# Performance work log

Measured on AMD Instinct MI355X. Metric: run time of the kernel, lower is better.

## Reference

```python
import jax, jax.numpy as jnp
import numpy as np

EPS = 1e-5

def _layernorm(x, gamma, beta, axes):
    mean = jnp.mean(x, axis=axes, keepdims=True)
    var = jnp.var(x, axis=axes, keepdims=True)
    return (x - mean) * jax.lax.rsqrt(var + EPS) * gamma + beta

def setup_inputs() -> dict:
    key = jax.random.key(0)
    ks = jax.random.split(key, 14)
    B, N1, N2, D1, D2 = 128, 32, 32, 23, 13
    E, H, F = 72, 256, 128
    N = N1 + N2
    s = 0.05
    return {
        "x_a": jax.random.normal(ks[0], (B, N1, D1), jnp.float32),
        "x_b": jax.random.normal(ks[1], (B, N2, D2), jnp.float32),
        "W_a": jax.random.normal(ks[2], (D1, E), jnp.float32) * s,
        "b_a": jnp.zeros((E,), jnp.float32),
        "W_b": jax.random.normal(ks[3], (D2, E), jnp.float32) * s,
        "b_b": jnp.zeros((E,), jnp.float32),
        "ln0_g": jnp.ones((N, E), jnp.float32),
        "ln0_b": jnp.zeros((N, E), jnp.float32),
        "W_g": jax.random.normal(ks[4], (2 * E, H), jnp.float32) * s,
        "b_g": jnp.zeros((H,), jnp.float32),
        "lng_g": jnp.ones((H,), jnp.float32),
        "lng_b": jnp.zeros((H,), jnp.float32),
        "W_f": jax.random.normal(ks[5], (H, F), jnp.float32) * s,
        "b_f": jnp.zeros((F,), jnp.float32),
    }

def reference(x_a, x_b, W_a, b_a, W_b, b_b, ln0_g, ln0_b,
              W_g, b_g, lng_g, lng_b, W_f, b_f):
    # SplitEmbedding: per-group linear embed, concat along entity dim
    a = jnp.concatenate([x_a @ W_a + b_a, x_b @ W_b + b_b], axis=-2)  # [B, N, E]
    # LayerNorm over last two dims (num_entities, embed_dim) jointly
    a = _layernorm(a, ln0_g, ln0_b, axes=(-2, -1))
    B, N, E = a.shape
    # ij(): aij[b, i, j] = concat(a[b, i], a[b, j])  -> [B, N, N, 2E]
    ai = jnp.broadcast_to(a[:, :, None, :], (B, N, N, E))
    aj = jnp.broadcast_to(a[:, None, :, :], (B, N, N, E))
    aij = jnp.concatenate([ai, aj], axis=-1)
    # g: Linear(2E, H) + ELU, then LayerNorm(H)
    g = jax.nn.elu(aij @ W_g + b_g)  # [B, N, N, H]
    g = _layernorm(g, lng_g, lng_b, axes=(-1,))
    # sum over both pairwise dims
    s = jnp.sum(g, axis=(-3, -2))  # [B, H]
    # f: Linear(H, F) + ELU
    return jax.nn.elu(s @ W_f + b_f)  # [B, F]
```

## Files before the change

### kernel.cpp

```cpp
#include <hip/hip_runtime.h>
#include <hip/hip_bf16.h>

#define EPS 1e-5f
#define LOG2E 1.44269504088896f
#define LN2   0.69314718055995f

typedef float v2f __attribute__((ext_vector_type(2)));

#define OFF_ABAR 0
#define OFF_U    589824
#define OFF_V    2686976
#define OFF_PART 4784128

__device__ __forceinline__ float elu(float z) {
    return z > 0.f ? z : __expf(z) - 1.f;
}

__global__ __launch_bounds__(256) void k_embed_ln0(
    const float* __restrict__ xa, const float* __restrict__ xb,
    const float* __restrict__ Wa, const float* __restrict__ ba,
    const float* __restrict__ Wb, const float* __restrict__ bb,
    const float* __restrict__ g0, const float* __restrict__ b0,
    float* __restrict__ abar) {
    int b = blockIdx.x;
    int tid = threadIdx.x;
    __shared__ float S[3888];
    float* s_xa = S;
    float* s_xb = S + 736;
    float* s_Wa = S + 1152;
    float* s_Wb = S + 2808;
    float* s_ba = S + 3744;
    float* s_bb = S + 3816;
    for (int k = tid; k < 736;  k += 256) s_xa[k] = xa[b * 736 + k];
    for (int k = tid; k < 416;  k += 256) s_xb[k] = xb[b * 416 + k];
    for (int k = tid; k < 1656; k += 256) s_Wa[k] = Wa[k];
    for (int k = tid; k < 936;  k += 256) s_Wb[k] = Wb[k];
    if (tid < 72) { s_ba[tid] = ba[tid]; s_bb[tid] = bb[tid]; }
    __syncthreads();

    float vals[18];
    float s1 = 0.f, s2 = 0.f;
    #pragma unroll
    for (int m = 0; m < 18; ++m) {
        int k = tid + 256 * m;
        int e = k % 72;
        int n = k / 72;
        float acc;
        if (n < 32) {
            acc = s_ba[e];
            const float* x = s_xa + n * 23;
            #pragma unroll
            for (int d = 0; d < 23; ++d) acc = fmaf(x[d], s_Wa[d * 72 + e], acc);
        } else {
            acc = s_bb[e];
            const float* x = s_xb + (n - 32) * 13;
            #pragma unroll
            for (int d = 0; d < 13; ++d) acc = fmaf(x[d], s_Wb[d * 72 + e], acc);
        }
        vals[m] = acc;
        s1 += acc;
        s2 = fmaf(acc, acc, s2);
    }
    #pragma unroll
    for (int off = 32; off >= 1; off >>= 1) {
        s1 += __shfl_xor(s1, off, 64);
        s2 += __shfl_xor(s2, off, 64);
    }
    __shared__ float r1[4], r2[4];
    int w = tid >> 6;
    if ((tid & 63) == 0) { r1[w] = s1; r2[w] = s2; }
    __syncthreads();
    float t1 = r1[0] + r1[1] + r1[2] + r1[3];
    float t2 = r2[0] + r2[1] + r2[2] + r2[3];
    float mean = t1 * (1.f / 4608.f);
    float var  = fmaf(-mean, mean, t2 * (1.f / 4608.f));
    float rsq  = rsqrtf(var + EPS);
    float* ab = abar + b * 4608;
    #pragma unroll
    for (int m = 0; m < 18; ++m) {
        int k = tid + 256 * m;
        ab[k] = fmaf((vals[m] - mean) * rsq, g0[k], b0[k]);
    }
}

__global__ __launch_bounds__(256) void k_uv(
    const float* __restrict__ abar, const float* __restrict__ Wg,
    const float* __restrict__ bg,
    float* __restrict__ U, float* __restrict__ V) {
    int blk = blockIdx.x;
    int b = blk >> 3;
    int q = blk & 7;
    int h = threadIdx.x;
    __shared__ float sa[72 * 8];
    const float* src = abar + (b * 64 + q * 8) * 72;
    for (int k = threadIdx.x; k < 72 * 8; k += 256) {
        int e = k >> 3, n = k & 7;
        sa[k] = src[n * 72 + e];
    }
    __syncthreads();
    float u[8], v[8];
    #pragma unroll
    for (int n = 0; n < 8; ++n) { u[n] = 0.f; v[n] = 0.f; }
    #pragma unroll 6
    for (int e = 0; e < 72; ++e) {
        float wu = Wg[e * 256 + h];
        float wv = Wg[(72 + e) * 256 + h];
        const float4* sp = (const float4*)&sa[e * 8];
        #pragma unroll
        for (int n4 = 0; n4 < 2; ++n4) {
            float4 s4 = sp[n4];
            u[n4*4+0] = fmaf(s4.x, wu, u[n4*4+0]); v[n4*4+0] = fmaf(s4.x, wv, v[n4*4+0]);
            u[n4*4+1] = fmaf(s4.y, wu, u[n4*4+1]); v[n4*4+1] = fmaf(s4.y, wv, v[n4*4+1]);
            u[n4*4+2] = fmaf(s4.z, wu, u[n4*4+2]); v[n4*4+2] = fmaf(s4.z, wv, v[n4*4+2]);
            u[n4*4+3] = fmaf(s4.w, wu, u[n4*4+3]); v[n4*4+3] = fmaf(s4.w, wv, v[n4*4+3]);
        }
    }
    float bgh = bg[h];
    int base = (b * 64 + q * 8) * 256 + h;
    #pragma unroll
    for (int n = 0; n < 8; ++n) {
        U[base + n * 256] = u[n] + bgh;
        V[base + n * 256] = v[n];
    }
}

__global__ __launch_bounds__(256) void k_pair(
    const float* __restrict__ U, const float* __restrict__ V,
    float* __restrict__ part) {
    int blk = blockIdx.x;
    int b  = blk >> 5;
    int iq = (blk >> 2) & 7;
    int jq = blk & 3;
    int t  = threadIdx.x;
    int j16 = t >> 4;
    int hc  = t & 15;

    __shared__ float Us[16 * 256];

    const float* Ug = U + (size_t)(b * 64 + iq * 8) * 256;
    #pragma unroll
    for (int r = 0; r < 2; ++r) {
        int k = t * 4 + r * 1024;
        *(float4*)&Us[k] = *(const float4*)&Ug[k];
    }

    const float* Vrow = V + (size_t)(b * 64 + jq * 16 + j16) * 256;
    v2f v[8];
    #pragma unroll
    for (int c = 0; c < 4; ++c) {
        float4 v4 = *(const float4*)&Vrow[hc * 4 + 64 * c];
        v[2*c]   = (v2f){v4.x, v4.y};
        v[2*c+1] = (v2f){v4.z, v4.w};
    }

    __syncthreads();

    v2f acc[8];
    #pragma unroll
    for (int k = 0; k < 8; ++k) acc[k] = (v2f){0.f, 0.f};
    float macc = 0.f;

    #pragma unroll 2
    for (int i = 0; i < 8; ++i) {
        const float* ur = &Us[i * 256];
        v2f e[8];
        v2f s1v = (v2f){0.f, 0.f};
        v2f s2v = (v2f){0.f, 0.f};
        #pragma unroll
        for (int c = 0; c < 8; ++c) {
            float2 u2 = *(const float2*)&ur[hc * 4 + 32 * c + (c & 1) * 0];
            (void)u2;
        }
        #pragma unroll
        for (int c = 0; c < 4; ++c) {
            float4 u4 = *(const float4*)&ur[hc * 4 + 64 * c];
            v2f z0 = (v2f){u4.x, u4.y} + v[2*c];
            v2f z1 = (v2f){u4.z, u4.w} + v[2*c+1];
            v2f zl0 = z0 * (v2f){LOG2E, LOG2E};
            v2f zl1 = z1 * (v2f){LOG2E, LOG2E};
            v2f e0, e1;
            e0.x = zl0.x > 0.f ? z0.x : __builtin_amdgcn_exp2f(zl0.x) - 1.f;
            e0.y = zl0.y > 0.f ? z0.y : __builtin_amdgcn_exp2f(zl0.y) - 1.f;
            e1.x = zl1.x > 0.f ? z1.x : __builtin_amdgcn_exp2f(zl1.x) - 1.f;
            e1.y = zl1.y > 0.f ? z1.y : __builtin_amdgcn_exp2f(zl1.y) - 1.f;
            e[2*c] = e0; e[2*c+1] = e1;
            s1v += e0 + e1;
            s2v = e0 * e0 + s2v;
            s2v = e1 * e1 + s2v;
        }
        float s1 = s1v.x + s1v.y;
        float s2 = s2v.x + s2v.y;
        #pragma unroll
        for (int d = 1; d <= 8; d <<= 1) {
            s1 += __shfl_xor(s1, d, 64);
            s2 += __shfl_xor(s2, d, 64);
        }
        float mu  = s1 * (1.f / 256.f);
        float var = fmaf(-mu, mu, s2 * (1.f / 256.f));
        float rsq = rsqrtf(var + EPS);
        macc += mu * rsq;
        v2f r2 = (v2f){rsq, rsq};
        #pragma unroll
        for (int k = 0; k < 8; ++k) acc[k] = e[k] * r2 + acc[k];
    }
    v2f m2 = (v2f){macc, macc};
    #pragma unroll
    for (int k = 0; k < 8; ++k) acc[k] -= m2;

    __syncthreads();
    #pragma unroll
    for (int c = 0; c < 4; ++c)
        *(float4*)&Us[j16 * 256 + hc * 4 + 64 * c] =
            make_float4(acc[2*c].x, acc[2*c].y, acc[2*c+1].x, acc[2*c+1].y);
    __syncthreads();
    float r = 0.f;
    #pragma unroll
    for (int q = 0; q < 16; ++q) r += Us[q * 256 + t];
    part[(size_t)blk * 256 + t] = r;
}

__global__ __launch_bounds__(512) void k_out(
    const float* __restrict__ part,
    const float* __restrict__ lgg, const float* __restrict__ lgb,
    const float* __restrict__ Wf,  const float* __restrict__ bfb,
    float* __restrict__ out) {
    int b = blockIdx.x;
    int t = threadIdx.x;
    __shared__ float sh[256];
    __shared__ float ps[512];
    {
        int h = t & 255, pg = t >> 8;
        float s = 0.f;
        #pragma unroll
        for (int p = 0; p < 16; ++p)
            s += part[(size_t)(b * 32 + pg * 16 + p) * 256 + h];
        ps[t] = s;
    }
    __syncthreads();
    if (t < 256) sh[t] = fmaf(lgg[t], ps[t] + ps[t + 256], 4096.f * lgb[t]);
    __syncthreads();
    {
        int f = t & 127, hq = t >> 7;
        float acc = 0.f;
        #pragma unroll 8
        for (int h = hq * 64; h < hq * 64 + 64; ++h)
            acc = fmaf(sh[h], Wf[h * 128 + f], acc);
        ps[t] = acc;
    }
    __syncthreads();
    if (t < 128) {
        float r = ps[t] + ps[t + 128] + ps[t + 256] + ps[t + 384] + bfb[t];
        out[b * 128 + t] = r > 0.f ? r : __expf(r) - 1.f;
    }
}

extern "C" void kernel_launch(void* const* d_in, const int* in_sizes, int n_in,
                              void* d_out, int out_size, void* d_ws, size_t ws_size,
                              hipStream_t stream) {
    const float* xa  = (const float*)d_in[0];
    const float* xb  = (const float*)d_in[1];
    const float* Wa  = (const float*)d_in[2];
    const float* ba  = (const float*)d_in[3];
    const float* Wb  = (const float*)d_in[4];
    const float* bb  = (const float*)d_in[5];
    const float* g0  = (const float*)d_in[6];
    const float* b0  = (const float*)d_in[7];
    const float* Wg  = (const float*)d_in[8];
    const float* bg  = (const float*)d_in[9];
    const float* lgg = (const float*)d_in[10];
    const float* lgb = (const float*)d_in[11];
    const float* Wf  = (const float*)d_in[12];
    const float* bfb = (const float*)d_in[13];
    float* out = (float*)d_out;

    float* ws   = (float*)d_ws;
    float* abar = ws + OFF_ABAR;
    float* U    = ws + OFF_U;
    float* V    = ws + OFF_V;
    float* part = ws + OFF_PART;

    k_embed_ln0<<<128, 256, 0, stream>>>(xa, xb, Wa, ba, Wb, bb, g0, b0, abar);
    k_uv<<<1024, 256, 0, stream>>>(abar, Wg, bg, U, V);
    k_pair<<<4096, 256, 0, stream>>>(U, V, part);
    k_out<<<128, 512, 0, stream>>>(part, lgg, lgb, Wf, bfb, out);
}
```

Before: 145.0 us.

## Fuse embedding+LayerNorm into U/V projection kernel, recomputing per block

Merges the embedding/LN0 kernel into the U/V projection kernel. Each of the 1024 blocks recomputes the full per-batch embedding and LayerNorm statistics, then keeps only its 8 entities in shared memory. This removes one kernel launch and the global round trip of the normalized activations. In exchange the embedding work is done 8 times redundantly. It also deletes a dead load loop in the pair kernel.

```diff
diff --git a/kernel.cpp b/kernel.cpp
--- a/kernel.cpp
+++ b/kernel.cpp
@@ -16,15 +16,21 @@
     return z > 0.f ? z : __expf(z) - 1.f;
 }
 
-__global__ __launch_bounds__(256) void k_embed_ln0(
+__global__ __launch_bounds__(256) void k_embed_uv(
     const float* __restrict__ xa, const float* __restrict__ xb,
     const float* __restrict__ Wa, const float* __restrict__ ba,
     const float* __restrict__ Wb, const float* __restrict__ bb,
     const float* __restrict__ g0, const float* __restrict__ b0,
-    float* __restrict__ abar) {
-    int b = blockIdx.x;
+    const float* __restrict__ Wg, const float* __restrict__ bg,
+    float* __restrict__ U, float* __restrict__ V) {
+    int blk = blockIdx.x;
+    int b = blk >> 3;
+    int q = blk & 7;
     int tid = threadIdx.x;
+
     __shared__ float S[3888];
+    __shared__ float sa[72 * 8];
+    __shared__ float r1[4], r2[4];
     float* s_xa = S;
     float* s_xb = S + 736;
     float* s_Wa = S + 1152;
@@ -66,7 +72,6 @@
         s1 += __shfl_xor(s1, off, 64);
         s2 += __shfl_xor(s2, off, 64);
     }
-    __shared__ float r1[4], r2[4];
     int w = tid >> 6;
     if ((tid & 63) == 0) { r1[w] = s1; r2[w] = s2; }
     __syncthreads();
@@ -75,29 +80,20 @@
     float mean = t1 * (1.f / 4608.f);
     float var  = fmaf(-mean, mean, t2 * (1.f / 4608.f));
     float rsq  = rsqrtf(var + EPS);
-    float* ab = abar + b * 4608;
+
+    int n0 = q * 8;
     #pragma unroll
     for (int m = 0; m < 18; ++m) {
         int k = tid + 256 * m;
-        ab[k] = fmaf((vals[m] - mean) * rsq, g0[k], b0[k]);
-    }
-}
-
-__global__ __launch_bounds__(256) void k_uv(
-    const float* __restrict__ abar, const float* __restrict__ Wg,
-    const float* __restrict__ bg,
-    float* __restrict__ U, float* __restrict__ V) {
-    int blk = blockIdx.x;
-    int b = blk >> 3;
-    int q = blk & 7;
-    int h = threadIdx.x;
-    __shared__ float sa[72 * 8];
-    const float* src = abar + (b * 64 + q * 8) * 72;
-    for (int k = threadIdx.x; k < 72 * 8; k += 256) {
-        int e = k >> 3, n = k & 7;
-        sa[k] = src[n * 72 + e];
-    }
-    __syncthreads();
+        int dn = k / 72 - n0;
+        if ((unsigned)dn < 8u) {
+            int e = k % 72;
+            sa[e * 8 + dn] = fmaf((vals[m] - mean) * rsq, g0[k], b0[k]);
+        }
+    }
+    __syncthreads();
+
+    int h = tid;
     float u[8], v[8];
     #pragma unroll
     for (int n = 0; n < 8; ++n) { u[n] = 0.f; v[n] = 0.f; }
@@ -116,7 +112,7 @@
         }
     }
     float bgh = bg[h];
-    int base = (b * 64 + q * 8) * 256 + h;
+    int base = (b * 64 + n0) * 256 + h;
     #pragma unroll
     for (int n = 0; n < 8; ++n) {
         U[base + n * 256] = u[n] + bgh;
@@ -166,11 +162,6 @@
         v2f e[8];
         v2f s1v = (v2f){0.f, 0.f};
         v2f s2v = (v2f){0.f, 0.f};
-        #pragma unroll
-        for (int c = 0; c < 8; ++c) {
-            float2 u2 = *(const float2*)&ur[hc * 4 + 32 * c + (c & 1) * 0];
-            (void)u2;
-        }
         #pragma unroll
         for (int c = 0; c < 4; ++c) {
             float4 u4 = *(const float4*)&ur[hc * 4 + 64 * c];
@@ -274,13 +265,12 @@
     float* out = (float*)d_out;
 
     float* ws   = (float*)d_ws;
-    float* abar = ws + OFF_ABAR;
     float* U    = ws + OFF_U;
     float* V    = ws + OFF_V;
     float* part = ws + OFF_PART;
 
-    k_embed_ln0<<<128, 256, 0, stream>>>(xa, xb, Wa, ba, Wb, bb, g0, b0, abar);
-    k_uv<<<1024, 256, 0, stream>>>(abar, Wg, bg, U, V);
+    k_embed_uv<<<1024, 256, 0, stream>>>(xa, xb, Wa, ba, Wb, bb, g0, b0,
+                                         Wg, bg, U, V);
     k_pair<<<4096, 256, 0, stream>>>(U, V, part);
     k_out<<<128, 512, 0, stream>>>(part, lgg, lgb, Wf, bfb, out);
 }
```

Result: slower. 175.0 us (+20.7%).

## Fuse output stage into pair kernel via last-block-done atomic counter

Applied to the files above, without the earlier changes.

Removes the separate k_out launch. Each k_pair block now increments a per-batch counter after writing its partial sums, and the last of the 32 blocks for that batch reduces the partials and applies the LayerNorm affine, the final linear layer and ELU. The counters are zeroed in the first kernel. It also deletes a dead shared-memory load loop. This saves one kernel launch and its tail, at the cost of an atomic and threadfences in every pair block, and the final matvec now runs serially in a single 256-thread block per batch.

```diff
diff --git a/kernel.cpp b/kernel.cpp
--- a/kernel.cpp
+++ b/kernel.cpp
@@ -11,6 +11,7 @@
 #define OFF_U    589824
 #define OFF_V    2686976
 #define OFF_PART 4784128
+#define OFF_CNT  5832704
 
 __device__ __forceinline__ float elu(float z) {
     return z > 0.f ? z : __expf(z) - 1.f;
@@ -21,9 +22,10 @@
     const float* __restrict__ Wa, const float* __restrict__ ba,
     const float* __restrict__ Wb, const float* __restrict__ bb,
     const float* __restrict__ g0, const float* __restrict__ b0,
-    float* __restrict__ abar) {
+    float* __restrict__ abar, unsigned* __restrict__ cnt) {
     int b = blockIdx.x;
     int tid = threadIdx.x;
+    if (tid == 0) cnt[b] = 0u;
     __shared__ float S[3888];
     float* s_xa = S;
     float* s_xb = S + 736;
@@ -126,7 +128,10 @@
 
 __global__ __launch_bounds__(256) void k_pair(
     const float* __restrict__ U, const float* __restrict__ V,
-    float* __restrict__ part) {
+    float* __restrict__ part, unsigned* __restrict__ cnt,
+    const float* __restrict__ lgg, const float* __restrict__ lgb,
+    const float* __restrict__ Wf,  const float* __restrict__ bfb,
+    float* __restrict__ out) {
     int blk = blockIdx.x;
     int b  = blk >> 5;
     int iq = (blk >> 2) & 7;
@@ -166,11 +171,6 @@
         v2f e[8];
         v2f s1v = (v2f){0.f, 0.f};
         v2f s2v = (v2f){0.f, 0.f};
-        #pragma unroll
-        for (int c = 0; c < 8; ++c) {
-            float2 u2 = *(const float2*)&ur[hc * 4 + 32 * c + (c & 1) * 0];
-            (void)u2;
-        }
         #pragma unroll
         for (int c = 0; c < 4; ++c) {
             float4 u4 = *(const float4*)&ur[hc * 4 + 64 * c];
@@ -217,40 +217,31 @@
     #pragma unroll
     for (int q = 0; q < 16; ++q) r += Us[q * 256 + t];
     part[(size_t)blk * 256 + t] = r;
-}
-
-__global__ __launch_bounds__(512) void k_out(
-    const float* __restrict__ part,
-    const float* __restrict__ lgg, const float* __restrict__ lgb,
-    const float* __restrict__ Wf,  const float* __restrict__ bfb,
-    float* __restrict__ out) {
-    int b = blockIdx.x;
-    int t = threadIdx.x;
-    __shared__ float sh[256];
-    __shared__ float ps[512];
-    {
-        int h = t & 255, pg = t >> 8;
+
+    __threadfence();
+    __shared__ unsigned s_prev;
+    if (t == 0) s_prev = atomicAdd(&cnt[b], 1u);
+    __syncthreads();
+    if (s_prev == 31u) {
+        __threadfence();
         float s = 0.f;
-        #pragma unroll
-        for (int p = 0; p < 16; ++p)
-            s += part[(size_t)(b * 32 + pg * 16 + p) * 256 + h];
-        ps[t] = s;
-    }
-    __syncthreads();
-    if (t < 256) sh[t] = fmaf(lgg[t], ps[t] + ps[t + 256], 4096.f * lgb[t]);
-    __syncthreads();
-    {
+        const float* pb = part + (size_t)(b * 32) * 256 + t;
+        #pragma unroll 8
+        for (int p = 0; p < 32; ++p) s += pb[(size_t)p * 256];
+        Us[t] = fmaf(lgg[t], s, 4096.f * lgb[t]);
+        __syncthreads();
         int f = t & 127, hq = t >> 7;
-        float acc = 0.f;
+        float accf = 0.f;
         #pragma unroll 8
-        for (int h = hq * 64; h < hq * 64 + 64; ++h)
-            acc = fmaf(sh[h], Wf[h * 128 + f], acc);
-        ps[t] = acc;
-    }
-    __syncthreads();
-    if (t < 128) {
-        float r = ps[t] + ps[t + 128] + ps[t + 256] + ps[t + 384] + bfb[t];
-        out[b * 128 + t] = r > 0.f ? r : __expf(r) - 1.f;
+        for (int h = hq * 128; h < hq * 128 + 128; ++h)
+            accf = fmaf(Us[h], Wf[h * 128 + f], accf);
+        __syncthreads();
+        Us[256 + t] = accf;
+        __syncthreads();
+        if (t < 128) {
+            float rr = Us[256 + t] + Us[256 + t + 128] + bfb[t];
+            out[b * 128 + t] = elu(rr);
+        }
     }
 }
 
@@ -278,9 +269,11 @@
     float* U    = ws + OFF_U;
     float* V    = ws + OFF_V;
     float* part = ws + OFF_PART;
-
-    k_embed_ln0<<<128, 256, 0, stream>>>(xa, xb, Wa, ba, Wb, bb, g0, b0, abar);
+    unsigned* cnt = (unsigned*)(ws + OFF_CNT);
+
+    k_embed_ln0<<<128, 256, 0, stream>>>(xa, xb, Wa, ba, Wb, bb, g0, b0,
+                                         abar, cnt);
     k_uv<<<1024, 256, 0, stream>>>(abar, Wg, bg, U, V);
-    k_pair<<<4096, 256, 0, stream>>>(U, V, part);
-    k_out<<<128, 512, 0, stream>>>(part, lgg, lgb, Wf, bfb, out);
-}
+    k_pair<<<4096, 256, 0, stream>>>(U, V, part, cnt,
+                                     lgg, lgb, Wf, bfb, out);
+}
```

Result: slower. 496.2 us (+242.2%).
